# Optimization experiments

Hardware: AMD Instinct MI355X
Metric: run time of the kernel (lower is better)

Reference implementation:

```python
import jax, jax.numpy as jnp
import numpy as np


def _log_g(x):
    # log_g(x) = log(relu(x)+1) if x >= 0 else x
    return jnp.where(x >= 0, jnp.log1p(jnp.maximum(x, 0.0)), x)


def _min_gru(hg):
    # hg: [B, H, L] -> [B, H/2, L]
    h, gate = jnp.split(hg, 2, axis=1)
    log_coeffs = -jax.nn.softplus(gate)                    # log(1 - z)
    log_values = -jax.nn.softplus(-gate) + _log_g(h)       # log(z) + log g(h)
    a_star = jnp.cumsum(log_coeffs, axis=2)
    log_h0_plus_b_star = jax.lax.cumlogsumexp(log_values - a_star, axis=2)
    return jnp.exp(a_star + log_h0_plus_b_star)


def setup_inputs() -> dict:
    key = jax.random.key(0)
    B, H, L = 8, 512, 8192
    x = jax.random.normal(key, (B, H, L), dtype=jnp.float32)
    return {"x": x}


def reference(x) -> jnp.ndarray:
    # bidirectional minGRU: forward scan on first half of channels,
    # reversed scan on second half.
    fore, back = jnp.split(x, 2, axis=1)
    out_fore = _min_gru(fore)
    out_back = jnp.flip(_min_gru(jnp.flip(back, axis=2)), axis=2)
    return jnp.concatenate([out_fore, out_back], axis=1)  # [B, H/2, L]
```

## Files before the change

### kernel.cpp

```cpp
#include <hip/hip_runtime.h>
#include <math.h>


#define SEQ_L 8192
#define NTHREADS 256
#define PER_THREAD 8
#define TILE (NTHREADS * PER_THREAD)
#define NTILES (SEQ_L / TILE)

__global__ __launch_bounds__(NTHREADS) void mingru_scan_kernel(
    const float* __restrict__ x, float* __restrict__ out) {
    const int blk = blockIdx.x;
    const int dir = blk >> 10;
    const int s   = blk & 1023;
    const int b   = s >> 7;
    const int c   = s & 127;

    const int tid  = threadIdx.x;
    const int lane = tid & 63;
    const int wave = tid >> 6;

    const float* __restrict__ hrow = x + (size_t)((b * 512) + (dir * 256) + c) * SEQ_L;
    const float* __restrict__ grow = hrow + (size_t)128 * SEQ_L;
    float* __restrict__ orow = out + (size_t)((b * 256) + (dir * 128) + c) * SEQ_L;

    __shared__ float sA[2][4];
    __shared__ float sB[2][4];

    float carry = 0.0f;

    {
    }
    int base0 = tid * PER_THREAD;
    int idx0  = dir ? (SEQ_L - base0 - PER_THREAD) : base0;
    float4 nh0 = *(const float4*)(hrow + idx0);
    float4 nh1 = *(const float4*)(hrow + idx0 + 4);
    float4 ng0 = *(const float4*)(grow + idx0);
    float4 ng1 = *(const float4*)(grow + idx0 + 4);

#pragma unroll
    for (int t = 0; t < NTILES; ++t) {
        const float4 h0 = nh0, h1 = nh1, g0 = ng0, g1 = ng1;

        if (t + 1 < NTILES) {
            const int nb = (t + 1) * TILE + tid * PER_THREAD;
            const int ni = dir ? (SEQ_L - nb - PER_THREAD) : nb;
            nh0 = *(const float4*)(hrow + ni);
            nh1 = *(const float4*)(hrow + ni + 4);
            ng0 = *(const float4*)(grow + ni);
            ng1 = *(const float4*)(grow + ni + 4);
        }

        float hv[PER_THREAD], gv[PER_THREAD];
        if (dir == 0) {
            hv[0]=h0.x; hv[1]=h0.y; hv[2]=h0.z; hv[3]=h0.w;
            hv[4]=h1.x; hv[5]=h1.y; hv[6]=h1.z; hv[7]=h1.w;
            gv[0]=g0.x; gv[1]=g0.y; gv[2]=g0.z; gv[3]=g0.w;
            gv[4]=g1.x; gv[5]=g1.y; gv[6]=g1.z; gv[7]=g1.w;
        } else {
            hv[0]=h1.w; hv[1]=h1.z; hv[2]=h1.y; hv[3]=h1.x;
            hv[4]=h0.w; hv[5]=h0.z; hv[6]=h0.y; hv[7]=h0.x;
            gv[0]=g1.w; gv[1]=g1.z; gv[2]=g1.y; gv[3]=g1.x;
            gv[4]=g0.w; gv[5]=g0.z; gv[6]=g0.y; gv[7]=g0.x;
        }

        float pp[PER_THREAD], ov0[PER_THREAD];
        float ca = 1.0f, cb = 0.0f;
#pragma unroll
        for (int j = 0; j < PER_THREAD; ++j) {
            const float gt = gv[j];
            const float e  = __expf(-fabsf(gt));
            const float r  = 1.0f / (1.0f + e);
            const float sn = e * r;
            const float z  = (gt >= 0.0f) ? r  : sn;
            const float a  = (gt >= 0.0f) ? sn : r;
            const float hh = hv[j];
            const float gf = (hh >= 0.0f) ? (hh + 1.0f) : __expf(hh);
            const float bb = z * gf;
            cb = a * cb + bb;
            ca = a * ca;
            ov0[j] = cb;
            pp[j]  = ca;
        }

        float pa = ca, pb = cb;
#pragma unroll
        for (int d = 1; d < 64; d <<= 1) {
            const float oa = __shfl_up(pa, d);
            const float ob = __shfl_up(pb, d);
            if (lane >= d) {
                pb = pa * ob + pb;
                pa = pa * oa;
            }
        }

        const int buf = t & 1;
        if (lane == 63) { sA[buf][wave] = pa; sB[buf][wave] = pb; }
        __syncthreads();

        float st = carry;
        for (int w = 0; w < wave; ++w) st = sA[buf][w] * st + sB[buf][w];
        float ea = __shfl_up(pa, 1);
        float eb = __shfl_up(pb, 1);
        if (lane == 0) { ea = 1.0f; eb = 0.0f; }
        st = ea * st + eb;

        float ov[PER_THREAD];
#pragma unroll
        for (int j = 0; j < PER_THREAD; ++j) ov[j] = ov0[j] + st * pp[j];

        const int base = t * TILE + tid * PER_THREAD;
        if (dir == 0) {
            *(float4*)(orow + base)     = make_float4(ov[0], ov[1], ov[2], ov[3]);
            *(float4*)(orow + base + 4) = make_float4(ov[4], ov[5], ov[6], ov[7]);
        } else {
            const int p = SEQ_L - base - PER_THREAD;
            *(float4*)(orow + p)     = make_float4(ov[7], ov[6], ov[5], ov[4]);
            *(float4*)(orow + p + 4) = make_float4(ov[3], ov[2], ov[1], ov[0]);
        }

        float nc = carry;
#pragma unroll
        for (int w = 0; w < 4; ++w) nc = sA[buf][w] * nc + sB[buf][w];
        carry = nc;
    }
}

extern "C" void kernel_launch(void* const* d_in, const int* in_sizes, int n_in,
                              void* d_out, int out_size, void* d_ws, size_t ws_size,
                              hipStream_t stream) {
    const float* x = (const float*)d_in[0];
    float* out = (float*)d_out;
    mingru_scan_kernel<<<2048, NTHREADS, 0, stream>>>(x, out);
}
```

Measured before the change: 209.6 us.

## Template scan on direction, simplify sigmoid math, use nontemporal stores

Turns the per-sequence scan into a function templated on direction, so the direction branches are resolved at compile time. The gate math is reduced to one exp and a hardware reciprocal (a = 1/(1+e^g), z = e*a), computed unconditionally. Explicit FMAs are used throughout, outputs go out through nontemporal stores, and launch bounds request 8 blocks per CU. This trims ALU work and cache pollution in a kernel that is mostly memory-bound. The unguarded exp(g) can overflow to inf for large gates and give NaN where the old stable form did not.

```diff
diff --git a/kernel.cpp b/kernel.cpp
--- a/kernel.cpp
+++ b/kernel.cpp
@@ -8,35 +8,22 @@
 #define TILE (NTHREADS * PER_THREAD)
 #define NTILES (SEQ_L / TILE)
 
-__global__ __launch_bounds__(NTHREADS) void mingru_scan_kernel(
-    const float* __restrict__ x, float* __restrict__ out) {
-    const int blk = blockIdx.x;
-    const int dir = blk >> 10;
-    const int s   = blk & 1023;
-    const int b   = s >> 7;
-    const int c   = s & 127;
+typedef float vf4 __attribute__((ext_vector_type(4)));
 
-    const int tid  = threadIdx.x;
-    const int lane = tid & 63;
-    const int wave = tid >> 6;
-
-    const float* __restrict__ hrow = x + (size_t)((b * 512) + (dir * 256) + c) * SEQ_L;
-    const float* __restrict__ grow = hrow + (size_t)128 * SEQ_L;
-    float* __restrict__ orow = out + (size_t)((b * 256) + (dir * 128) + c) * SEQ_L;
-
-    __shared__ float sA[2][4];
-    __shared__ float sB[2][4];
-
+template<int DIR>
+__device__ __forceinline__ void run_seq(const float* __restrict__ hrow,
+                                        const float* __restrict__ grow,
+                                        float* __restrict__ orow,
+                                        const int tid, const int lane, const int wave,
+                                        float (&sA)[2][4], float (&sB)[2][4]) {
     float carry = 0.0f;
 
-    {
-    }
-    int base0 = tid * PER_THREAD;
-    int idx0  = dir ? (SEQ_L - base0 - PER_THREAD) : base0;
-    float4 nh0 = *(const float4*)(hrow + idx0);
-    float4 nh1 = *(const float4*)(hrow + idx0 + 4);
-    float4 ng0 = *(const float4*)(grow + idx0);
-    float4 ng1 = *(const float4*)(grow + idx0 + 4);
+    const int b0 = tid * PER_THREAD;
+    const int i0 = DIR ? (SEQ_L - b0 - PER_THREAD) : b0;
+    float4 nh0 = *(const float4*)(hrow + i0);
+    float4 nh1 = *(const float4*)(hrow + i0 + 4);
+    float4 ng0 = *(const float4*)(grow + i0);
+    float4 ng1 = *(const float4*)(grow + i0 + 4);
 
 #pragma unroll
     for (int t = 0; t < NTILES; ++t) {
@@ -44,7 +31,7 @@
 
         if (t + 1 < NTILES) {
             const int nb = (t + 1) * TILE + tid * PER_THREAD;
-            const int ni = dir ? (SEQ_L - nb - PER_THREAD) : nb;
+            const int ni = DIR ? (SEQ_L - nb - PER_THREAD) : nb;
             nh0 = *(const float4*)(hrow + ni);
             nh1 = *(const float4*)(hrow + ni + 4);
             ng0 = *(const float4*)(grow + ni);
@@ -52,7 +39,7 @@
         }
 
         float hv[PER_THREAD], gv[PER_THREAD];
-        if (dir == 0) {
+        if (DIR == 0) {
             hv[0]=h0.x; hv[1]=h0.y; hv[2]=h0.z; hv[3]=h0.w;
             hv[4]=h1.x; hv[5]=h1.y; hv[6]=h1.z; hv[7]=h1.w;
             gv[0]=g0.x; gv[1]=g0.y; gv[2]=g0.z; gv[3]=g0.w;
@@ -68,17 +55,15 @@
         float ca = 1.0f, cb = 0.0f;
 #pragma unroll
         for (int j = 0; j < PER_THREAD; ++j) {
-            const float gt = gv[j];
-            const float e  = __expf(-fabsf(gt));
-            const float r  = 1.0f / (1.0f + e);
-            const float sn = e * r;
-            const float z  = (gt >= 0.0f) ? r  : sn;
-            const float a  = (gt >= 0.0f) ? sn : r;
+            const float e  = __expf(gv[j]);
+            const float a  = __builtin_amdgcn_rcpf(1.0f + e);
+            const float z  = e * a;
             const float hh = hv[j];
-            const float gf = (hh >= 0.0f) ? (hh + 1.0f) : __expf(hh);
+            const float eh = __expf(hh);
+            const float gf = (hh >= 0.0f) ? (hh + 1.0f) : eh;
             const float bb = z * gf;
-            cb = a * cb + bb;
-            ca = a * ca;
+            cb = fmaf(a, cb, bb);
+            ca *= a;
             ov0[j] = cb;
             pp[j]  = ca;
         }
@@ -89,8 +74,8 @@
             const float oa = __shfl_up(pa, d);
             const float ob = __shfl_up(pb, d);
             if (lane >= d) {
-                pb = pa * ob + pb;
-                pa = pa * oa;
+                pb = fmaf(pa, ob, pb);
+                pa *= oa;
             }
         }
 
@@ -99,31 +84,58 @@
         __syncthreads();
 
         float st = carry;
-        for (int w = 0; w < wave; ++w) st = sA[buf][w] * st + sB[buf][w];
+        for (int w = 0; w < wave; ++w) st = fmaf(sA[buf][w], st, sB[buf][w]);
         float ea = __shfl_up(pa, 1);
         float eb = __shfl_up(pb, 1);
         if (lane == 0) { ea = 1.0f; eb = 0.0f; }
-        st = ea * st + eb;
-
-        float ov[PER_THREAD];
-#pragma unroll
-        for (int j = 0; j < PER_THREAD; ++j) ov[j] = ov0[j] + st * pp[j];
+        st = fmaf(ea, st, eb);
 
         const int base = t * TILE + tid * PER_THREAD;
-        if (dir == 0) {
-            *(float4*)(orow + base)     = make_float4(ov[0], ov[1], ov[2], ov[3]);
-            *(float4*)(orow + base + 4) = make_float4(ov[4], ov[5], ov[6], ov[7]);
+        if (DIR == 0) {
+            vf4 o0 = { fmaf(st, pp[0], ov0[0]), fmaf(st, pp[1], ov0[1]),
+                       fmaf(st, pp[2], ov0[2]), fmaf(st, pp[3], ov0[3]) };
+            vf4 o1 = { fmaf(st, pp[4], ov0[4]), fmaf(st, pp[5], ov0[5]),
+                       fmaf(st, pp[6], ov0[6]), fmaf(st, pp[7], ov0[7]) };
+            __builtin_nontemporal_store(o0, (vf4*)(orow + base));
+            __builtin_nontemporal_store(o1, (vf4*)(orow + base + 4));
         } else {
             const int p = SEQ_L - base - PER_THREAD;
-            *(float4*)(orow + p)     = make_float4(ov[7], ov[6], ov[5], ov[4]);
-            *(float4*)(orow + p + 4) = make_float4(ov[3], ov[2], ov[1], ov[0]);
+            vf4 o0 = { fmaf(st, pp[7], ov0[7]), fmaf(st, pp[6], ov0[6]),
+                       fmaf(st, pp[5], ov0[5]), fmaf(st, pp[4], ov0[4]) };
+            vf4 o1 = { fmaf(st, pp[3], ov0[3]), fmaf(st, pp[2], ov0[2]),
+                       fmaf(st, pp[1], ov0[1]), fmaf(st, pp[0], ov0[0]) };
+            __builtin_nontemporal_store(o0, (vf4*)(orow + p));
+            __builtin_nontemporal_store(o1, (vf4*)(orow + p + 4));
         }
 
         float nc = carry;
 #pragma unroll
-        for (int w = 0; w < 4; ++w) nc = sA[buf][w] * nc + sB[buf][w];
+        for (int w = 0; w < 4; ++w) nc = fmaf(sA[buf][w], nc, sB[buf][w]);
         carry = nc;
     }
+}
+
+__global__ __launch_bounds__(NTHREADS, 8) void mingru_scan_kernel(
+    const float* __restrict__ x, float* __restrict__ out) {
+    const int blk = blockIdx.x;
+    const int dir = blk >> 10;
+    const int s   = blk & 1023;
+    const int b   = s >> 7;
+    const int c   = s & 127;
+
+    const int tid  = threadIdx.x;
+    const int lane = tid & 63;
+    const int wave = tid >> 6;
+
+    const float* hrow = x + (size_t)((b * 512) + (dir * 256) + c) * SEQ_L;
+    const float* grow = hrow + (size_t)128 * SEQ_L;
+    float* orow = out + (size_t)((b * 256) + (dir * 128) + c) * SEQ_L;
+
+    __shared__ float sA[2][4];
+    __shared__ float sB[2][4];
+
+    if (dir == 0) run_seq<0>(hrow, grow, orow, tid, lane, wave, sA, sB);
+    else          run_seq<1>(hrow, grow, orow, tid, lane, wave, sA, sB);
 }
 
 extern "C" void kernel_launch(void* const* d_in, const int* in_sizes, int n_in,
```

Result: slower. 222.5 us (+6.2%).
